# Performance work log

Hardware: AMD Instinct MI355X
Metric: run time of the kernel (lower is better)

Reference implementation:

```python
import jax, jax.numpy as jnp
import numpy as np

B, L, D, N, F, V, NL, NS = 2, 1024, 768, 16, 3072, 32000, 4, 3
EPS = 1e-5


def _layernorm(x, g, b):
    m = x.mean(-1, keepdims=True)
    v = ((x - m) ** 2).mean(-1, keepdims=True)
    return (x - m) / jnp.sqrt(v + EPS) * g + b


def _ssm_sublayer(x, cw, A_log, WB, WC, Wdt, dtb, Dsk):
    # x: [B,L,D]; causal depthwise conv, kernel_size=3
    xp = jnp.pad(x, ((0, 0), (2, 0), (0, 0)))
    u = xp[:, :-2] * cw[:, 0] + xp[:, 1:-1] * cw[:, 1] + xp[:, 2:] * cw[:, 2]
    u = jax.nn.silu(u)
    dt = jax.nn.softplus(jnp.einsum('bld,de->ble', u, Wdt) + dtb)   # [B,L,D]
    Bm = jnp.einsum('bld,dn->bln', u, WB)                           # [B,L,N]
    Cm = jnp.einsum('bld,dn->bln', u, WC)                           # [B,L,N]
    A = -jnp.exp(A_log)                                             # [D,N]

    def step(h, t):
        dt_t, u_t, b_t, c_t = t                                     # [B,D],[B,D],[B,N],[B,N]
        h = jnp.exp(dt_t[..., None] * A) * h + (dt_t * u_t)[..., None] * b_t[:, None, :]
        y = jnp.einsum('bdn,bn->bd', h, c_t)
        return h, y

    h0 = jnp.zeros((x.shape[0], x.shape[2], A.shape[1]), x.dtype)
    _, ys = jax.lax.scan(step, h0, (dt.transpose(1, 0, 2), u.transpose(1, 0, 2),
                                    Bm.transpose(1, 0, 2), Cm.transpose(1, 0, 2)))
    return ys.transpose(1, 0, 2) + Dsk * u


def setup_inputs() -> dict:
    key = jax.random.key(0)
    ks = jax.random.split(key, 16)
    g = lambda k, shape, s=0.02: jax.random.normal(k, shape, jnp.float32) * s
    inp = {
        'x': jax.random.randint(ks[0], (B, L), 0, V),
        'emb': g(ks[1], (V, D)),
        'conv_w': g(ks[2], (NL, NS, D, 3), 0.2),
        'A_log': jnp.log(jnp.tile(jnp.arange(1, N + 1, dtype=jnp.float32), (NL, NS, D, 1))),
        'W_B': g(ks[3], (NL, NS, D, N)),
        'W_C': g(ks[4], (NL, NS, D, N)),
        'W_dt': g(ks[5], (NL, NS, D, D)),
        'dt_bias': jnp.full((NL, NS, D), -4.0, jnp.float32),
        'D_skip': jnp.ones((NL, NS, D), jnp.float32),
        'ffn_W1': g(ks[6], (NL, D, F)),
        'ffn_b1': jnp.zeros((NL, F), jnp.float32),
        'ffn_W2': g(ks[7], (NL, F, D)),
        'ffn_b2': jnp.zeros((NL, D), jnp.float32),
        'norm_g': jnp.ones((D,), jnp.float32),
        'norm_b': jnp.zeros((D,), jnp.float32),
        'out_W': g(ks[8], (D, V)),
        'out_b': jnp.zeros((V,), jnp.float32),
    }
    return inp


def reference(x, emb, conv_w, A_log, W_B, W_C, W_dt, dt_bias, D_skip,
              ffn_W1, ffn_b1, ffn_W2, ffn_b2, norm_g, norm_b, out_W, out_b):
    h = emb[x]                                                      # [B,L,D]
    for l in range(NL):
        for s in range(NS):
            h = h + _ssm_sublayer(h, conv_w[l, s], A_log[l, s], W_B[l, s],
                                  W_C[l, s], W_dt[l, s], dt_bias[l, s], D_skip[l, s])
        f = jax.nn.gelu(jnp.einsum('bld,df->blf', h, ffn_W1[l]) + ffn_b1[l], approximate=False)
        h = h + jnp.einsum('blf,fd->bld', f, ffn_W2[l]) + ffn_b2[l]
    h = _layernorm(h, norm_g, norm_b)
    logits = jnp.einsum('bld,dv->blv', h, out_W) + out_b            # [B,L,V]
    return logits
```

## Files before the change

### kernel.cpp

```cpp
#include <hip/hip_runtime.h>
#include <hip/hip_bf16.h>
#include <math.h>

#define BB 2
#define LL 1024
#define DD 768
#define NN 16
#define FF 3072
#define VV 32000
#define NLL 4
#define NSS 3
#define BL (BB*LL)
#define CHK 64
#define CLEN (LL/CHK)

typedef __bf16 bf16x8 __attribute__((ext_vector_type(8)));
typedef float f32x4 __attribute__((ext_vector_type(4)));
typedef short short8 __attribute__((ext_vector_type(8)));

typedef __attribute__((address_space(1))) const void gconst_t;
typedef __attribute__((address_space(3))) void lds_t;

__device__ __forceinline__ void g2l16(const void* g, void* l) {
  __builtin_amdgcn_global_load_lds((gconst_t*)g, (lds_t*)l, 16, 0, 0);
}



__global__ __launch_bounds__(256) void k_embed(
    const int* __restrict__ x, const float* __restrict__ emb,
    float* __restrict__ h) {
  int row = blockIdx.x;
  int idx = x[row];
  const float* e = emb + (size_t)idx * DD;
  float* hr = h + (size_t)row * DD;
  int t = threadIdx.x;
  hr[t]       = e[t];
  hr[t + 256] = e[t + 256];
  hr[t + 512] = e[t + 512];
}

__global__ __launch_bounds__(256) void k_conv(
    const float* __restrict__ h, const float* __restrict__ cw,
    __hip_bfloat16* __restrict__ ub) {
  int row = blockIdx.x;
  int l = row & (LL - 1);
  #pragma unroll
  for (int d = threadIdx.x; d < DD; d += 256) {
    float w0 = cw[d * 3 + 0], w1 = cw[d * 3 + 1], w2 = cw[d * 3 + 2];
    float v = h[(size_t)row * DD + d] * w2;
    if (l >= 1) v += h[(size_t)(row - 1) * DD + d] * w1;
    if (l >= 2) v += h[(size_t)(row - 2) * DD + d] * w0;
    float sv = v / (1.f + __expf(-v));
    ub[(size_t)row * DD + d] = __float2bfloat16(sv);
  }
}

__global__ __launch_bounds__(256) void k_layernorm(
    const float* __restrict__ x, const float* __restrict__ g,
    const float* __restrict__ bta, __hip_bfloat16* __restrict__ o) {
  int row = blockIdx.x;
  const float* xr = x + (size_t)row * DD;
  int tid = threadIdx.x;
  float v1 = xr[tid], v2 = xr[tid + 256], v3 = xr[tid + 512];
  float s = v1 + v2 + v3;
  float sq = v1 * v1 + v2 * v2 + v3 * v3;
  #pragma unroll
  for (int m = 1; m < 64; m <<= 1) {
    s  += __shfl_xor(s, m);
    sq += __shfl_xor(sq, m);
  }
  __shared__ float ss[4], sqs[4];
  if ((tid & 63) == 0) { ss[tid >> 6] = s; sqs[tid >> 6] = sq; }
  __syncthreads();
  s  = ss[0] + ss[1] + ss[2] + ss[3];
  sq = sqs[0] + sqs[1] + sqs[2] + sqs[3];
  float mean = s * (1.f / DD);
  float var  = sq * (1.f / DD) - mean * mean;
  float rstd = rsqrtf(var + 1e-5f);
  o[(size_t)row * DD + tid]       = __float2bfloat16((v1 - mean) * rstd * g[tid]       + bta[tid]);
  o[(size_t)row * DD + tid + 256] = __float2bfloat16((v2 - mean) * rstd * g[tid + 256] + bta[tid + 256]);
  o[(size_t)row * DD + tid + 512] = __float2bfloat16((v3 - mean) * rstd * g[tid + 512] + bta[tid + 512]);
}

#define S1 1728
#define S2 1740
#define S3 4044
#define S4 6348
#define SEND 12348

__global__ __launch_bounds__(256) void k_wconv_all(
    const float* __restrict__ Wdt, const float* __restrict__ WB,
    const float* __restrict__ WC, const float* __restrict__ W1,
    const float* __restrict__ W2, const float* __restrict__ Wout,
    __hip_bfloat16* __restrict__ WTdt, __hip_bfloat16* __restrict__ WT1,
    __hip_bfloat16* __restrict__ WT2, __hip_bfloat16* __restrict__ WTlog) {
  __shared__ float T[64][65];
  int bid = blockIdx.x;
  int tid = threadIdx.x;

  if (bid >= S1 && bid < S2) {
    int sub = bid - S1;
    const float* WBp = WB + (size_t)sub * DD * NN;
    const float* WCp = WC + (size_t)sub * DD * NN;
    __hip_bfloat16* dst = WTdt + (size_t)sub * 832 * DD;
    for (int e = tid; e < 64 * DD; e += 256) {
      int r = e / DD, k = e - (e / DD) * DD;
      float v = 0.f;
      if (r < 16)      v = WBp[(size_t)k * NN + r];
      else if (r < 32) v = WCp[(size_t)k * NN + (r - 16)];
      dst[(size_t)(768 + r) * DD + k] = __float2bfloat16(v);
    }
    return;
  }

  const float* W; __hip_bfloat16* WT;
  int K, N, n0, k0;
  if (bid < S1) {
    int sub = bid / 144, t = bid % 144;
    W = Wdt + (size_t)sub * DD * DD; WT = WTdt + (size_t)sub * 832 * DD;
    K = DD; N = DD; n0 = (t % 12) * 64; k0 = (t / 12) * 64;
  } else if (bid < S3) {
    int idx = bid - S2, l = idx / 576, t = idx % 576;
    W = W1 + (size_t)l * DD * FF; WT = WT1 + (size_t)l * FF * DD;
    K = DD; N = FF; n0 = (t % 48) * 64; k0 = (t / 48) * 64;
  } else if (bid < S4) {
    int idx = bid - S3, l = idx / 576, t = idx % 576;
    W = W2 + (size_t)l * FF * DD; WT = WT2 + (size_t)l * DD * FF;
    K = FF; N = DD; n0 = (t % 12) * 64; k0 = (t / 12) * 64;
  } else {
    int t = bid - S4;
    W = Wout; WT = WTlog;
    K = DD; N = VV; n0 = (t % 500) * 64; k0 = (t / 500) * 64;
  }

  int c = tid & 63, r4 = tid >> 6;
  #pragma unroll
  for (int i = 0; i < 16; ++i) {
    int k_l = r4 + i * 4;
    T[k_l][c] = W[(size_t)(k0 + k_l) * N + n0 + c];
  }
  __syncthreads();
  #pragma unroll
  for (int i = 0; i < 16; ++i) {
    int n_l = r4 + i * 4;
    WT[(size_t)(n0 + n_l) * K + k0 + c] = __float2bfloat16(T[c][n_l]);
  }
}

__device__ __forceinline__ float softplus_f(float x) {
  return (x > 20.f) ? x : log1pf(__expf(x));
}
__device__ __forceinline__ float gelu_f(float x) {
  return 0.5f * x * (1.f + erff(x * 0.70710678118654752f));
}

__global__ __launch_bounds__(256) void k_gemm_ffn1(
    const __hip_bfloat16* __restrict__ A, const __hip_bfloat16* __restrict__ BT,
    const float* __restrict__ bias, __hip_bfloat16* __restrict__ Cb) {
  __shared__ __align__(16) __hip_bfloat16 As[128 * 64];
  __shared__ __align__(16) __hip_bfloat16 Bs[128 * 64];
  const int tid = threadIdx.x;
  const int lane = tid & 63, wid = tid >> 6;
  int wg = (blockIdx.x & 7) * 48 + (blockIdx.x >> 3);
  int tn = wg % 24, tm = wg / 24;
  const int bm = tm * 128, bn = tn * 128;
  const int wm = wid >> 1, wn = wid & 1;
  const int sr = lane >> 3;
  const int sks = (((lane & 7) ^ (lane >> 3)) & 7) * 8;
  const int N = FF, K = DD;

  f32x4 acc[4][4] = {};

  for (int k0 = 0; k0 < K; k0 += 64) {
    __syncthreads();
    #pragma unroll
    for (int cc = 0; cc < 4; ++cc) {
      int ch = wid * 4 + cc;
      int row = ch * 8 + sr;
      g2l16(A  + (size_t)(bm + row) * K + k0 + sks, &As[ch * 512]);
      g2l16(BT + (size_t)(bn + row) * K + k0 + sks, &Bs[ch * 512]);
    }
    __syncthreads();
    #pragma unroll
    for (int kk = 0; kk < 2; ++kk) {
      int koff = (((kk * 4 + (lane >> 4)) ^ (lane & 7)) & 7) * 8;
      bf16x8 af[4], bfr[4];
      #pragma unroll
      for (int m = 0; m < 4; ++m)
        af[m] = *(const bf16x8*)&As[(wm * 64 + m * 16 + (lane & 15)) * 64 + koff];
      #pragma unroll
      for (int n = 0; n < 4; ++n)
        bfr[n] = *(const bf16x8*)&Bs[(wn * 64 + n * 16 + (lane & 15)) * 64 + koff];
      #pragma unroll
      for (int m = 0; m < 4; ++m)
        #pragma unroll
        for (int n = 0; n < 4; ++n)
          acc[m][n] = __builtin_amdgcn_mfma_f32_16x16x32_bf16(af[m], bfr[n], acc[m][n], 0, 0, 0);
    }
  }

  const int crow0 = (lane >> 4) * 4;
  const int ccol = lane & 15;
  #pragma unroll
  for (int m = 0; m < 4; ++m) {
    #pragma unroll
    for (int n = 0; n < 4; ++n) {
      int col = bn + wn * 64 + n * 16 + ccol;
      float bv = bias[col];
      #pragma unroll
      for (int j = 0; j < 4; ++j) {
        int row = bm + wm * 64 + m * 16 + crow0 + j;
        Cb[(size_t)row * N + col] = __float2bfloat16(gelu_f(acc[m][n][j] + bv));
      }
    }
  }
}

__global__ __launch_bounds__(256) void k_gemm_dtbc64(
    const __hip_bfloat16* __restrict__ A, const __hip_bfloat16* __restrict__ BT,
    const float* __restrict__ dtbias, __hip_bfloat16* __restrict__ dtbb,
    float* __restrict__ Bm, float* __restrict__ Cm) {
  __shared__ __align__(16) __hip_bfloat16 As[64 * 64];
  __shared__ __align__(16) __hip_bfloat16 Bs[64 * 64];
  const int tid = threadIdx.x;
  const int lane = tid & 63, wid = tid >> 6;
  int wg = (blockIdx.x & 7) * 52 + (blockIdx.x >> 3);
  int tn = wg % 13, tm = wg / 13;
  const int bm = tm * 64, bn = tn * 64;
  const int wm = wid >> 1, wn = wid & 1;
  const int sr = lane >> 3;
  const int sks = (((lane & 7) ^ (lane >> 3)) & 7) * 8;

  f32x4 acc[2][2] = {};

  for (int k0 = 0; k0 < DD; k0 += 64) {
    __syncthreads();
    #pragma unroll
    for (int cc = 0; cc < 2; ++cc) {
      int ch = wid * 2 + cc;
      int row = ch * 8 + sr;
      g2l16(A  + (size_t)(bm + row) * DD + k0 + sks, &As[ch * 512]);
      g2l16(BT + (size_t)(bn + row) * DD + k0 + sks, &Bs[ch * 512]);
    }
    __syncthreads();
    #pragma unroll
    for (int kk = 0; kk < 2; ++kk) {
      int koff = (((kk * 4 + (lane >> 4)) ^ (lane & 7)) & 7) * 8;
      bf16x8 af[2], bfr[2];
      #pragma unroll
      for (int m = 0; m < 2; ++m)
        af[m] = *(const bf16x8*)&As[(wm * 32 + m * 16 + (lane & 15)) * 64 + koff];
      #pragma unroll
      for (int n = 0; n < 2; ++n)
        bfr[n] = *(const bf16x8*)&Bs[(wn * 32 + n * 16 + (lane & 15)) * 64 + koff];
      #pragma unroll
      for (int m = 0; m < 2; ++m)
        #pragma unroll
        for (int n = 0; n < 2; ++n)
          acc[m][n] = __builtin_amdgcn_mfma_f32_16x16x32_bf16(af[m], bfr[n], acc[m][n], 0, 0, 0);
    }
  }

  const int crow0 = (lane >> 4) * 4;
  const int ccol = lane & 15;
  #pragma unroll
  for (int m = 0; m < 2; ++m) {
    #pragma unroll
    for (int n = 0; n < 2; ++n) {
      int col = bn + wn * 32 + n * 16 + ccol;
      if (col >= 800) continue;
      float bv = (col < DD) ? dtbias[col] : 0.f;
      #pragma unroll
      for (int j = 0; j < 4; ++j) {
        int row = bm + wm * 32 + m * 16 + crow0 + j;
        float v = acc[m][n][j] + bv;
        if (col < DD)       dtbb[(size_t)row * DD + col] = __float2bfloat16(softplus_f(v));
        else if (col < 784) Bm[(size_t)row * NN + (col - DD)] = v;
        else                Cm[(size_t)row * NN + (col - 784)] = v;
      }
    }
  }
}

__global__ __launch_bounds__(256) void k_gemm_ffn2s(
    const __hip_bfloat16* __restrict__ A, const __hip_bfloat16* __restrict__ BT,
    const float* __restrict__ bias, float* __restrict__ h) {
  __shared__ __align__(16) __hip_bfloat16 As[64 * 64];
  __shared__ __align__(16) __hip_bfloat16 Bs[64 * 64];
  const int tid = threadIdx.x;
  const int lane = tid & 63, wid = tid >> 6;
  int wg = (blockIdx.x & 7) * 96 + (blockIdx.x >> 3);
  int tile = wg % 384, split = wg / 384;
  int tm = tile % 32, tn = tile / 32;
  const int bm = tm * 64, bn = tn * 64;
  const int wm = wid >> 1, wn = wid & 1;
  const int sr = lane >> 3;
  const int sks = (((lane & 7) ^ (lane >> 3)) & 7) * 8;
  const int kbeg = split * (FF / 2), kend = kbeg + FF / 2;

  f32x4 acc[2][2] = {};

  for (int k0 = kbeg; k0 < kend; k0 += 64) {
    __syncthreads();
    #pragma unroll
    for (int cc = 0; cc < 2; ++cc) {
      int ch = wid * 2 + cc;
      int row = ch * 8 + sr;
      g2l16(A  + (size_t)(bm + row) * FF + k0 + sks, &As[ch * 512]);
      g2l16(BT + (size_t)(bn + row) * FF + k0 + sks, &Bs[ch * 512]);
    }
    __syncthreads();
    #pragma unroll
    for (int kk = 0; kk < 2; ++kk) {
      int koff = (((kk * 4 + (lane >> 4)) ^ (lane & 7)) & 7) * 8;
      bf16x8 af[2], bfr[2];
      #pragma unroll
      for (int m = 0; m < 2; ++m)
        af[m] = *(const bf16x8*)&As[(wm * 32 + m * 16 + (lane & 15)) * 64 + koff];
      #pragma unroll
      for (int n = 0; n < 2; ++n)
        bfr[n] = *(const bf16x8*)&Bs[(wn * 32 + n * 16 + (lane & 15)) * 64 + koff];
      #pragma unroll
      for (int m = 0; m < 2; ++m)
        #pragma unroll
        for (int n = 0; n < 2; ++n)
          acc[m][n] = __builtin_amdgcn_mfma_f32_16x16x32_bf16(af[m], bfr[n], acc[m][n], 0, 0, 0);
    }
  }

  const int crow0 = (lane >> 4) * 4;
  const int ccol = lane & 15;
  #pragma unroll
  for (int m = 0; m < 2; ++m) {
    #pragma unroll
    for (int n = 0; n < 2; ++n) {
      int col = bn + wn * 32 + n * 16 + ccol;
      float bv = (split == 0) ? bias[col] : 0.f;
      #pragma unroll
      for (int j = 0; j < 4; ++j) {
        int row = bm + wm * 32 + m * 16 + crow0 + j;
        unsafeAtomicAdd(&h[(size_t)row * DD + col], acc[m][n][j] + bv);
      }
    }
  }
}

__global__ __launch_bounds__(512) void k_gemm_logits2(
    const __hip_bfloat16* __restrict__ A, const __hip_bfloat16* __restrict__ BT,
    const float* __restrict__ bias, float* __restrict__ C, int M, int N, int K) {
  __shared__ __align__(16) char smem[(256 * 64 + 128 * 64) * 2];
  __hip_bfloat16* As = (__hip_bfloat16*)smem;
  __hip_bfloat16* Bs = (__hip_bfloat16*)(smem + 256 * 64 * 2);
  const int tid = threadIdx.x;
  const int lane = tid & 63, wid = tid >> 6;
  int bid = blockIdx.y * gridDim.x + blockIdx.x;
  int mt = bid & 7, nt = bid >> 3;
  const int bm = mt * 256, bn = nt * 128;
  const int wm = wid >> 1, wn = wid & 1;
  const int sr = lane >> 3;
  const int sks = (((lane & 7) ^ (lane >> 3)) & 7) * 8;

  f32x4 acc[4][4] = {};

  for (int k0 = 0; k0 < K; k0 += 64) {
    __syncthreads();
    #pragma unroll
    for (int r = 0; r < 4; ++r) {
      int ch = r * 8 + wid;
      int row = ch * 8 + sr;
      g2l16(A + (size_t)(bm + row) * K + k0 + sks, &As[ch * 512]);
    }
    #pragma unroll
    for (int r = 0; r < 2; ++r) {
      int ch = r * 8 + wid;
      int row = ch * 8 + sr;
      g2l16(BT + (size_t)(bn + row) * K + k0 + sks, &Bs[ch * 512]);
    }
    __syncthreads();
    #pragma unroll
    for (int kk = 0; kk < 2; ++kk) {
      int koff = (((kk * 4 + (lane >> 4)) ^ (lane & 7)) & 7) * 8;
      bf16x8 af[4], bfr[4];
      #pragma unroll
      for (int m = 0; m < 4; ++m)
        af[m] = *(const bf16x8*)&As[(wm * 64 + m * 16 + (lane & 15)) * 64 + koff];
      #pragma unroll
      for (int n = 0; n < 4; ++n)
        bfr[n] = *(const bf16x8*)&Bs[(wn * 64 + n * 16 + (lane & 15)) * 64 + koff];
      #pragma unroll
      for (int m = 0; m < 4; ++m)
        #pragma unroll
        for (int n = 0; n < 4; ++n)
          acc[m][n] = __builtin_amdgcn_mfma_f32_16x16x32_bf16(af[m], bfr[n], acc[m][n], 0, 0, 0);
    }
  }

  __syncthreads();
  float* eps = (float*)smem + (size_t)wid * 1088;
  const int crow0 = (lane >> 4) * 4;
  const int ccol = lane & 15;
  const int gcolbase = bn + wn * 64;
  #pragma unroll
  for (int m = 0; m < 4; ++m) {
    #pragma unroll
    for (int n = 0; n < 4; ++n) {
      float bv = bias[gcolbase + n * 16 + ccol];
      #pragma unroll
      for (int j = 0; j < 4; ++j)
        eps[(crow0 + j) * 68 + n * 16 + ccol] = acc[m][n][j] + bv;
    }
    int growbase = bm + wm * 64 + m * 16;
    #pragma unroll
    for (int p = 0; p < 2; ++p) {
      int r = (lane >> 3) + 8 * p;
      #pragma unroll
      for (int i = 0; i < 2; ++i) {
        int s4 = (lane & 7) + 8 * i;
        float4 v = *(float4*)&eps[r * 68 + s4 * 4];
        *(float4*)&C[(size_t)(growbase + r) * N + gcolbase + s4 * 4] = v;
      }
    }
  }
}

__global__ __launch_bounds__(256) void k_scan_a(
    const __hip_bfloat16* __restrict__ dt, const __hip_bfloat16* __restrict__ ub,
    const float* __restrict__ Bm, const float* __restrict__ A_log,
    __hip_bfloat16* __restrict__ F, float* __restrict__ SD) {
  int c = blockIdx.x;
  int bd = blockIdx.y;
  int b = bd / 3;
  int d = (bd % 3) * 256 + threadIdx.x;
  float Av[16];
  {
    const float4* al = (const float4*)(A_log + (size_t)d * NN);
    #pragma unroll
    for (int q = 0; q < 4; ++q) {
      float4 v = al[q];
      Av[q * 4 + 0] = -__expf(v.x);
      Av[q * 4 + 1] = -__expf(v.y);
      Av[q * 4 + 2] = -__expf(v.z);
      Av[q * 4 + 3] = -__expf(v.w);
    }
  }
  float h[16];
  #pragma unroll
  for (int n = 0; n < 16; ++n) h[n] = 0.f;
  float sdt = 0.f;
  size_t base = ((size_t)b * LL + (size_t)c * CLEN) * DD + d;
  int row0 = c * CLEN + b * LL;
  #pragma unroll 4
  for (int t = 0; t < CLEN; ++t) {
    float dtv = __bfloat162float(dt[base + (size_t)t * DD]);
    float uv  = __bfloat162float(ub[base + (size_t)t * DD]);
    float Bv[16];
    const float4* bp = (const float4*)(Bm + (size_t)(row0 + t) * NN);
    *(float4*)&Bv[0]  = bp[0];
    *(float4*)&Bv[4]  = bp[1];
    *(float4*)&Bv[8]  = bp[2];
    *(float4*)&Bv[12] = bp[3];
    float du = dtv * uv;
    sdt += dtv;
    #pragma unroll
    for (int n = 0; n < 16; ++n)
      h[n] = __expf(dtv * Av[n]) * h[n] + du * Bv[n];
  }
  alignas(16) __hip_bfloat16 fx[16];
  #pragma unroll
  for (int n = 0; n < 16; ++n) fx[n] = __float2bfloat16(h[n]);
  __hip_bfloat16* fo = F + (((size_t)c * BB + b) * DD + d) * NN;
  *(short8*)&fo[0] = *(short8*)&fx[0];
  *(short8*)&fo[8] = *(short8*)&fx[8];
  SD[((size_t)c * BB + b) * DD + d] = sdt;
}

__global__ __launch_bounds__(256) void k_scan_b(
    const __hip_bfloat16* __restrict__ F, const float* __restrict__ SD,
    const float* __restrict__ A_log, __hip_bfloat16* __restrict__ Hinit) {
  __shared__ float Ls[64 * 17];
  __shared__ float Ho[64 * 17];
  __shared__ float Ss[64];
  int bd = blockIdx.x;
  int b = bd / DD, d = bd % DD;
  int tid = threadIdx.x;
  if (tid < 128) {
    int c = tid >> 1, q = tid & 1;
    alignas(16) __hip_bfloat16 fx[8];
    *(short8*)fx = *(const short8*)(F + (((size_t)c * BB + b) * DD + d) * NN + q * 8);
    #pragma unroll
    for (int i = 0; i < 8; ++i)
      Ls[c * 17 + q * 8 + i] = __bfloat162float(fx[i]);
  }
  if (tid < 64) Ss[tid] = SD[((size_t)tid * BB + b) * DD + d];
  __syncthreads();
  int lane = tid & 63, w = tid >> 6;
  #pragma unroll
  for (int r = 0; r < 4; ++r) {
    int n = w * 4 + r;
    float Av = -__expf(A_log[(size_t)d * NN + n]);
    float Fv = Ls[lane * 17 + n];
    float Dv = __expf(Ss[lane] * Av);
    #pragma unroll
    for (int s = 1; s < 64; s <<= 1) {
      float Fp = __shfl_up(Fv, s);
      float Dp = __shfl_up(Dv, s);
      float nF = Fv + Dv * Fp;
      float nD = Dv * Dp;
      Fv = (lane >= s) ? nF : Fv;
      Dv = (lane >= s) ? nD : Dv;
    }
    float Hi = __shfl_up(Fv, 1);
    if (lane == 0) Hi = 0.f;
    Ho[lane * 17 + n] = Hi;
  }
  __syncthreads();
  if (tid < 128) {
    int c = tid >> 1, q = tid & 1;
    alignas(16) __hip_bfloat16 hx[8];
    #pragma unroll
    for (int i = 0; i < 8; ++i)
      hx[i] = __float2bfloat16(Ho[c * 17 + q * 8 + i]);
    *(short8*)(Hinit + (((size_t)c * BB + b) * DD + d) * NN + q * 8) = *(short8*)hx;
  }
}

__global__ __launch_bounds__(256) void k_scan_c(
    const __hip_bfloat16* __restrict__ dt, const __hip_bfloat16* __restrict__ ub,
    const float* __restrict__ Bm, const float* __restrict__ Cm,
    const float* __restrict__ A_log, const float* __restrict__ Dsk,
    const __hip_bfloat16* __restrict__ Hinit, float* __restrict__ hres,
    __hip_bfloat16* __restrict__ hb, int writeHb) {
  int c = blockIdx.x;
  int bd = blockIdx.y;
  int b = bd / 3;
  int d = (bd % 3) * 256 + threadIdx.x;
  float Av[16];
  {
    const float4* al = (const float4*)(A_log + (size_t)d * NN);
    #pragma unroll
    for (int q = 0; q < 4; ++q) {
      float4 v = al[q];
      Av[q * 4 + 0] = -__expf(v.x);
      Av[q * 4 + 1] = -__expf(v.y);
      Av[q * 4 + 2] = -__expf(v.z);
      Av[q * 4 + 3] = -__expf(v.w);
    }
  }
  float h[16];
  {
    alignas(16) __hip_bfloat16 hx[16];
    const __hip_bfloat16* hi = Hinit + (((size_t)c * BB + b) * DD + d) * NN;
    *(short8*)&hx[0] = *(const short8*)&hi[0];
    *(short8*)&hx[8] = *(const short8*)&hi[8];
    #pragma unroll
    for (int n = 0; n < 16; ++n) h[n] = __bfloat162float(hx[n]);
  }
  float dskip = Dsk[d];
  size_t base = ((size_t)b * LL + (size_t)c * CLEN) * DD + d;
  int row0 = c * CLEN + b * LL;
  #pragma unroll 4
  for (int t = 0; t < CLEN; ++t) {
    float dtv = __bfloat162float(dt[base + (size_t)t * DD]);
    float uv  = __bfloat162float(ub[base + (size_t)t * DD]);
    float Bv[16], Cv[16];
    const float4* bp = (const float4*)(Bm + (size_t)(row0 + t) * NN);
    const float4* cp = (const float4*)(Cm + (size_t)(row0 + t) * NN);
    *(float4*)&Bv[0]  = bp[0];
    *(float4*)&Bv[4]  = bp[1];
    *(float4*)&Bv[8]  = bp[2];
    *(float4*)&Bv[12] = bp[3];
    *(float4*)&Cv[0]  = cp[0];
    *(float4*)&Cv[4]  = cp[1];
    *(float4*)&Cv[8]  = cp[2];
    *(float4*)&Cv[12] = cp[3];
    float du = dtv * uv;
    float y = 0.f;
    #pragma unroll
    for (int n = 0; n < 16; ++n) {
      h[n] = __expf(dtv * Av[n]) * h[n] + du * Bv[n];
      y += h[n] * Cv[n];
    }
    float nh = hres[base + (size_t)t * DD] + y + dskip * uv;
    hres[base + (size_t)t * DD] = nh;
    if (writeHb) hb[base + (size_t)t * DD] = __float2bfloat16(nh);
  }
}

extern "C" void kernel_launch(void* const* d_in, const int* in_sizes, int n_in,
                              void* d_out, int out_size, void* d_ws, size_t ws_size,
                              hipStream_t stream) {
  const int*   x     = (const int*)d_in[0];
  const float* emb   = (const float*)d_in[1];
  const float* convw = (const float*)d_in[2];
  const float* A_log = (const float*)d_in[3];
  const float* W_B   = (const float*)d_in[4];
  const float* W_C   = (const float*)d_in[5];
  const float* W_dt  = (const float*)d_in[6];
  const float* dt_b  = (const float*)d_in[7];
  const float* D_sk  = (const float*)d_in[8];
  const float* W1    = (const float*)d_in[9];
  const float* b1    = (const float*)d_in[10];
  const float* W2    = (const float*)d_in[11];
  const float* b2    = (const float*)d_in[12];
  const float* ng    = (const float*)d_in[13];
  const float* nb    = (const float*)d_in[14];
  const float* Wout  = (const float*)d_in[15];
  const float* bout  = (const float*)d_in[16];
  float* out = (float*)d_out;

  __hip_bfloat16* WTdt = (__hip_bfloat16*)d_out;
  __hip_bfloat16* WT1  = WTdt + (size_t)12 * 832 * DD;
  __hip_bfloat16* WT2  = WT1  + (size_t)NLL * FF * DD;

  char* p = (char*)d_ws;
  auto alloc = [&](size_t bytes) { char* r = p; p += (bytes + 255) & ~(size_t)255; return r; };
  float* h    = (float*)alloc((size_t)BL * DD * 4);
  float* Bm   = (float*)alloc((size_t)BL * NN * 4);
  float* Cm   = (float*)alloc((size_t)BL * NN * 4);
  float* SD   = (float*)alloc((size_t)CHK * BB * DD * 4);
  __hip_bfloat16* dtbb  = (__hip_bfloat16*)alloc((size_t)BL * DD * 2);
  __hip_bfloat16* F     = (__hip_bfloat16*)alloc((size_t)CHK * BB * DD * NN * 2);
  __hip_bfloat16* Hini  = (__hip_bfloat16*)alloc((size_t)CHK * BB * DD * NN * 2);
  __hip_bfloat16* ub    = (__hip_bfloat16*)alloc((size_t)BL * DD * 2);
  __hip_bfloat16* hb    = (__hip_bfloat16*)alloc((size_t)BL * DD * 2);
  __hip_bfloat16* fb    = (__hip_bfloat16*)alloc((size_t)BL * FF * 2);
  __hip_bfloat16* lnb   = (__hip_bfloat16*)alloc((size_t)BL * DD * 2);
  __hip_bfloat16* WTlog = (__hip_bfloat16*)alloc((size_t)VV * DD * 2);

  k_wconv_all<<<SEND, 256, 0, stream>>>(
      W_dt, W_B, W_C, W1, W2, Wout, WTdt, WT1, WT2, WTlog);
  k_embed<<<BL, 256, 0, stream>>>(x, emb, h);

  for (int l = 0; l < NLL; ++l) {
    for (int s = 0; s < NSS; ++s) {
      int ls = l * NSS + s;
      k_conv<<<BL, 256, 0, stream>>>(h, convw + (size_t)ls * DD * 3, ub);
      k_gemm_dtbc64<<<416, 256, 0, stream>>>(
          ub, WTdt + (size_t)ls * 832 * DD, dt_b + (size_t)ls * DD, dtbb, Bm, Cm);
      k_scan_a<<<dim3(CHK, 6), 256, 0, stream>>>(
          dtbb, ub, Bm, A_log + (size_t)ls * DD * NN, F, SD);
      k_scan_b<<<BB * DD, 256, 0, stream>>>(
          F, SD, A_log + (size_t)ls * DD * NN, Hini);
      k_scan_c<<<dim3(CHK, 6), 256, 0, stream>>>(
          dtbb, ub, Bm, Cm, A_log + (size_t)ls * DD * NN, D_sk + (size_t)ls * DD,
          Hini, h, hb, (s == NSS - 1) ? 1 : 0);
    }
    k_gemm_ffn1<<<384, 256, 0, stream>>>(
        hb, WT1 + (size_t)l * FF * DD, b1 + (size_t)l * FF, fb);
    k_gemm_ffn2s<<<768, 256, 0, stream>>>(
        fb, WT2 + (size_t)l * DD * FF, b2 + (size_t)l * DD, h);
  }

  k_layernorm<<<BL, 256, 0, stream>>>(h, ng, nb, lnb);
  k_gemm_logits2<<<dim3(VV / 128, BL / 256), 512, 0, stream>>>(
      lnb, WTlog, bout, out, BL, VV, DD);
}
```

Measured before the change: 1.133 ms.

## Vectorize conv and weight transpose, enlarge FFN2 tiles with split-K of four

The depthwise conv kernel now has each thread handle four channels, using float4 loads and a packed 8-byte bf16 store, and the grid is resized to match. The weight-convert transpose reads rows with float4 loads and writes bf16 in 16-byte chunks. The FFN2 GEMM moves from 64x64 tiles with split-K of two to 128x128 tiles with split-K of four, so each wave computes a 4x4 block of MFMA fragments and reuses more data from LDS. The larger tiles raise register and LDS use per block and halve the number of blocks, while the extra K splits increase atomic traffic to h.

```diff
diff --git a/kernel.cpp b/kernel.cpp
--- a/kernel.cpp
+++ b/kernel.cpp
@@ -17,6 +17,7 @@
 typedef __bf16 bf16x8 __attribute__((ext_vector_type(8)));
 typedef float f32x4 __attribute__((ext_vector_type(4)));
 typedef short short8 __attribute__((ext_vector_type(8)));
+typedef short short4v __attribute__((ext_vector_type(4)));
 
 typedef __attribute__((address_space(1))) const void gconst_t;
 typedef __attribute__((address_space(3))) void lds_t;
@@ -43,17 +44,29 @@
 __global__ __launch_bounds__(256) void k_conv(
     const float* __restrict__ h, const float* __restrict__ cw,
     __hip_bfloat16* __restrict__ ub) {
-  int row = blockIdx.x;
+  int gid = blockIdx.x * 256 + threadIdx.x;
+  int row = gid / 192;
+  int g = gid - row * 192;
+  int d0 = g * 4;
   int l = row & (LL - 1);
-  #pragma unroll
-  for (int d = threadIdx.x; d < DD; d += 256) {
-    float w0 = cw[d * 3 + 0], w1 = cw[d * 3 + 1], w2 = cw[d * 3 + 2];
-    float v = h[(size_t)row * DD + d] * w2;
-    if (l >= 1) v += h[(size_t)(row - 1) * DD + d] * w1;
-    if (l >= 2) v += h[(size_t)(row - 2) * DD + d] * w0;
+  float4 h0 = *(const float4*)&h[(size_t)row * DD + d0];
+  float4 h1, h2;
+  if (l >= 1) h1 = *(const float4*)&h[(size_t)(row - 1) * DD + d0];
+  else { h1.x = h1.y = h1.z = h1.w = 0.f; }
+  if (l >= 2) h2 = *(const float4*)&h[(size_t)(row - 2) * DD + d0];
+  else { h2.x = h2.y = h2.z = h2.w = 0.f; }
+  const float* hp0 = (const float*)&h0;
+  const float* hp1 = (const float*)&h1;
+  const float* hp2 = (const float*)&h2;
+  alignas(8) __hip_bfloat16 o[4];
+  #pragma unroll
+  for (int i = 0; i < 4; ++i) {
+    int d = d0 + i;
+    float v = hp2[i] * cw[d * 3 + 0] + hp1[i] * cw[d * 3 + 1] + hp0[i] * cw[d * 3 + 2];
     float sv = v / (1.f + __expf(-v));
-    ub[(size_t)row * DD + d] = __float2bfloat16(sv);
-  }
+    o[i] = __float2bfloat16(sv);
+  }
+  *(short4v*)&ub[(size_t)row * DD + d0] = *(short4v*)o;
 }
 
 __global__ __launch_bounds__(256) void k_layernorm(
@@ -134,17 +147,30 @@
     K = DD; N = VV; n0 = (t % 500) * 64; k0 = (t / 500) * 64;
   }
 
-  int c = tid & 63, r4 = tid >> 6;
-  #pragma unroll
-  for (int i = 0; i < 16; ++i) {
-    int k_l = r4 + i * 4;
-    T[k_l][c] = W[(size_t)(k0 + k_l) * N + n0 + c];
+  {
+    int r0 = tid >> 4, c4 = (tid & 15) * 4;
+    #pragma unroll
+    for (int i = 0; i < 4; ++i) {
+      int r = r0 + 16 * i;
+      float4 v = *(const float4*)&W[(size_t)(k0 + r) * N + n0 + c4];
+      T[r][c4 + 0] = v.x;
+      T[r][c4 + 1] = v.y;
+      T[r][c4 + 2] = v.z;
+      T[r][c4 + 3] = v.w;
+    }
   }
   __syncthreads();
-  #pragma unroll
-  for (int i = 0; i < 16; ++i) {
-    int n_l = r4 + i * 4;
-    WT[(size_t)(n0 + n_l) * K + k0 + c] = __float2bfloat16(T[c][n_l]);
+  {
+    int c8 = tid & 7;
+    #pragma unroll
+    for (int j = 0; j < 2; ++j) {
+      int n_l = (tid >> 3) + 32 * j;
+      alignas(16) __hip_bfloat16 ox[8];
+      #pragma unroll
+      for (int i = 0; i < 8; ++i)
+        ox[i] = __float2bfloat16(T[c8 * 8 + i][n_l]);
+      *(short8*)&WT[(size_t)(n0 + n_l) * K + k0 + c8 * 8] = *(short8*)ox;
+    }
   }
 }
 
@@ -286,26 +312,26 @@
 __global__ __launch_bounds__(256) void k_gemm_ffn2s(
     const __hip_bfloat16* __restrict__ A, const __hip_bfloat16* __restrict__ BT,
     const float* __restrict__ bias, float* __restrict__ h) {
-  __shared__ __align__(16) __hip_bfloat16 As[64 * 64];
-  __shared__ __align__(16) __hip_bfloat16 Bs[64 * 64];
+  __shared__ __align__(16) __hip_bfloat16 As[128 * 64];
+  __shared__ __align__(16) __hip_bfloat16 Bs[128 * 64];
   const int tid = threadIdx.x;
   const int lane = tid & 63, wid = tid >> 6;
-  int wg = (blockIdx.x & 7) * 96 + (blockIdx.x >> 3);
-  int tile = wg % 384, split = wg / 384;
-  int tm = tile % 32, tn = tile / 32;
-  const int bm = tm * 64, bn = tn * 64;
+  int wg = (blockIdx.x & 7) * 48 + (blockIdx.x >> 3);
+  int tile = wg % 96, split = wg / 96;
+  int tm = tile % 16, tn = tile / 16;
+  const int bm = tm * 128, bn = tn * 128;
   const int wm = wid >> 1, wn = wid & 1;
   const int sr = lane >> 3;
   const int sks = (((lane & 7) ^ (lane >> 3)) & 7) * 8;
-  const int kbeg = split * (FF / 2), kend = kbeg + FF / 2;
-
-  f32x4 acc[2][2] = {};
+  const int kbeg = split * (FF / 4), kend = kbeg + FF / 4;
+
+  f32x4 acc[4][4] = {};
 
   for (int k0 = kbeg; k0 < kend; k0 += 64) {
     __syncthreads();
     #pragma unroll
-    for (int cc = 0; cc < 2; ++cc) {
-      int ch = wid * 2 + cc;
+    for (int cc = 0; cc < 4; ++cc) {
+      int ch = wid * 4 + cc;
       int row = ch * 8 + sr;
       g2l16(A  + (size_t)(bm + row) * FF + k0 + sks, &As[ch * 512]);
       g2l16(BT + (size_t)(bn + row) * FF + k0 + sks, &Bs[ch * 512]);
@@ -314,17 +340,17 @@
     #pragma unroll
     for (int kk = 0; kk < 2; ++kk) {
       int koff = (((kk * 4 + (lane >> 4)) ^ (lane & 7)) & 7) * 8;
-      bf16x8 af[2], bfr[2];
-      #pragma unroll
-      for (int m = 0; m < 2; ++m)
-        af[m] = *(const bf16x8*)&As[(wm * 32 + m * 16 + (lane & 15)) * 64 + koff];
-      #pragma unroll
-      for (int n = 0; n < 2; ++n)
-        bfr[n] = *(const bf16x8*)&Bs[(wn * 32 + n * 16 + (lane & 15)) * 64 + koff];
-      #pragma unroll
-      for (int m = 0; m < 2; ++m)
+      bf16x8 af[4], bfr[4];
+      #pragma unroll
+      for (int m = 0; m < 4; ++m)
+        af[m] = *(const bf16x8*)&As[(wm * 64 + m * 16 + (lane & 15)) * 64 + koff];
+      #pragma unroll
+      for (int n = 0; n < 4; ++n)
+        bfr[n] = *(const bf16x8*)&Bs[(wn * 64 + n * 16 + (lane & 15)) * 64 + koff];
+      #pragma unroll
+      for (int m = 0; m < 4; ++m)
         #pragma unroll
-        for (int n = 0; n < 2; ++n)
+        for (int n = 0; n < 4; ++n)
           acc[m][n] = __builtin_amdgcn_mfma_f32_16x16x32_bf16(af[m], bfr[n], acc[m][n], 0, 0, 0);
     }
   }
@@ -332,14 +358,14 @@
   const int crow0 = (lane >> 4) * 4;
   const int ccol = lane & 15;
   #pragma unroll
-  for (int m = 0; m < 2; ++m) {
-    #pragma unroll
-    for (int n = 0; n < 2; ++n) {
-      int col = bn + wn * 32 + n * 16 + ccol;
+  for (int m = 0; m < 4; ++m) {
+    #pragma unroll
+    for (int n = 0; n < 4; ++n) {
+      int col = bn + wn * 64 + n * 16 + ccol;
       float bv = (split == 0) ? bias[col] : 0.f;
       #pragma unroll
       for (int j = 0; j < 4; ++j) {
-        int row = bm + wm * 32 + m * 16 + crow0 + j;
+        int row = bm + wm * 64 + m * 16 + crow0 + j;
         unsafeAtomicAdd(&h[(size_t)row * DD + col], acc[m][n][j] + bv);
       }
     }
@@ -635,7 +661,7 @@
   for (int l = 0; l < NLL; ++l) {
     for (int s = 0; s < NSS; ++s) {
       int ls = l * NSS + s;
-      k_conv<<<BL, 256, 0, stream>>>(h, convw + (size_t)ls * DD * 3, ub);
+      k_conv<<<1536, 256, 0, stream>>>(h, convw + (size_t)ls * DD * 3, ub);
       k_gemm_dtbc64<<<416, 256, 0, stream>>>(
           ub, WTdt + (size_t)ls * 832 * DD, dt_b + (size_t)ls * DD, dtbb, Bm, Cm);
       k_scan_a<<<dim3(CHK, 6), 256, 0, stream>>>(
@@ -648,7 +674,7 @@
     }
     k_gemm_ffn1<<<384, 256, 0, stream>>>(
         hb, WT1 + (size_t)l * FF * DD, b1 + (size_t)l * FF, fb);
-    k_gemm_ffn2s<<<768, 256, 0, stream>>>(
+    k_gemm_ffn2s<<<384, 256, 0, stream>>>(
         fb, WT2 + (size_t)l * DD * FF, b2 + (size_t)l * DD, h);
   }
 
```

New measurement: 1.154 ms. Within noise of the previous version (+1.9%).
